# Kernel tuning notes

Measured on AMD Instinct MI355X. Metric: run time of the kernel, lower is better.

The kernel has to match this reference:

```python
import jax, jax.numpy as jnp
import numpy as np

H = 768      # hidden_size
NH = 12      # num_attention_heads
DH = H // NH # attention_head_size
FF = 3072    # intermediate_size
E = 4        # n_expert
B, S = 8, 512
EPS = 1e-12


def _layernorm(x, g, b):
    mu = jnp.mean(x, axis=-1, keepdims=True)
    var = jnp.var(x, axis=-1, keepdims=True)
    return (x - mu) * jax.lax.rsqrt(var + EPS) * g + b


def _expert_linear(x, W, b, expert_idx):
    # W: [E, in, out], b: [E, out]; gather per-sample expert weights, then batched GEMM.
    # Mathematically identical to running every expert then slicing (single_select_fwd).
    Wg = W[expert_idx]            # [B, in, out]
    bg = b[expert_idx]            # [B, out]
    return jnp.einsum('bsi,bio->bso', x, Wg) + bg[:, None, :]


def setup_inputs() -> dict:
    key = jax.random.key(0)
    ks = jax.random.split(key, 16)
    sc = 0.02
    inp = {
        'hidden_states': jax.random.normal(ks[0], (B, S, H), jnp.float32),
        'expert_idx': jax.random.randint(ks[1], (B,), 0, E, jnp.int64) if jax.config.read('jax_enable_x64') else jax.random.randint(ks[1], (B,), 0, E).astype(jnp.int32),
        'attention_mask': jnp.zeros((B, 1, 1, S), jnp.float32),
        'Wq': sc * jax.random.normal(ks[2], (E, H, H), jnp.float32),
        'bq': jnp.zeros((E, H), jnp.float32),
        'Wk': sc * jax.random.normal(ks[3], (E, H, H), jnp.float32),
        'bk': jnp.zeros((E, H), jnp.float32),
        'Wv': sc * jax.random.normal(ks[4], (E, H, H), jnp.float32),
        'bv': jnp.zeros((E, H), jnp.float32),
        'Wo': sc * jax.random.normal(ks[5], (E, H, H), jnp.float32),
        'bo': jnp.zeros((E, H), jnp.float32),
        'ln1_g': jnp.ones((H,), jnp.float32),
        'ln1_b': jnp.zeros((H,), jnp.float32),
        'Wi': sc * jax.random.normal(ks[6], (E, H, FF), jnp.float32),
        'bi': jnp.zeros((E, FF), jnp.float32),
        'Wout': sc * jax.random.normal(ks[7], (E, FF, H), jnp.float32),
        'bout': jnp.zeros((E, H), jnp.float32),
        'ln2_g': jnp.ones((H,), jnp.float32),
        'ln2_b': jnp.zeros((H,), jnp.float32),
    }
    return inp


def reference(hidden_states, expert_idx, attention_mask, Wq, bq, Wk, bk, Wv, bv,
              Wo, bo, ln1_g, ln1_b, Wi, bi, Wout, bout, ln2_g, ln2_b):
    b, s, h = hidden_states.shape
    # --- MoE self-attention (per-sample expert QKV) ---
    q = _expert_linear(hidden_states, Wq, bq, expert_idx).reshape(b, s, NH, DH).transpose(0, 2, 1, 3)
    k = _expert_linear(hidden_states, Wk, bk, expert_idx).reshape(b, s, NH, DH).transpose(0, 2, 1, 3)
    v = _expert_linear(hidden_states, Wv, bv, expert_idx).reshape(b, s, NH, DH).transpose(0, 2, 1, 3)
    scores = jnp.einsum('bhqd,bhkd->bhqk', q, k) / np.sqrt(DH).astype(np.float32)
    scores = scores + attention_mask
    probs = jax.nn.softmax(scores, axis=-1)
    ctx = jnp.einsum('bhqk,bhkd->bhqd', probs, v).transpose(0, 2, 1, 3).reshape(b, s, h)
    # --- MoE self-output: dense + residual + LN ---
    attn_out = _expert_linear(ctx, Wo, bo, expert_idx)
    x = _layernorm(attn_out + hidden_states, ln1_g, ln1_b)
    # --- MoE FFN: intermediate (GELU) + output + residual + LN ---
    hmid = jax.nn.gelu(_expert_linear(x, Wi, bi, expert_idx), approximate=False)
    ffn = _expert_linear(hmid, Wout, bout, expert_idx)
    return _layernorm(ffn + x, ln2_g, ln2_b)
```

## Files before the change

### kernel.cpp

```cpp
#include <hip/hip_runtime.h>
#include <cstdint>
#include <cstddef>

constexpr int CB  = 8;
constexpr int CS  = 512;
constexpr int CH  = 768;
constexpr int CNH = 12;
constexpr int CDH = 64;
constexpr int CFF = 3072;
constexpr int CE  = 4;
constexpr int C3H = 3 * CH;

using f32x4  = __attribute__((ext_vector_type(4))) float;
using bf16x8 = __attribute__((ext_vector_type(8))) short;

__device__ __forceinline__ short f2bf(float x) {
  union { float f; uint32_t u; } v; v.f = x;
  return (short)((v.u + 0x7fffu + ((v.u >> 16) & 1u)) >> 16);
}

__device__ __forceinline__ void gload_lds16(const void* g, void* l) {
  __builtin_amdgcn_global_load_lds((const __attribute__((address_space(1))) void*)g,
                                   (__attribute__((address_space(3))) void*)l,
                                   16, 0, 0);
}

#define VMCNT(n)  asm volatile("s_waitcnt vmcnt(" #n ")" ::: "memory")
#define SCHEDB()  __builtin_amdgcn_sched_barrier(0)

__global__ void cvt_bf16_kernel(const float* __restrict__ in, short* __restrict__ out, int n4) {
  int i = blockIdx.x * blockDim.x + threadIdx.x;
  if (i < n4) {
    float4 v = ((const float4*)in)[i];
    short4 o;
    o.x = f2bf(v.x); o.y = f2bf(v.y); o.z = f2bf(v.z); o.w = f2bf(v.w);
    ((short4*)out)[i] = o;
  }
}

__device__ __forceinline__ bool expert_used(const int* __restrict__ eidx, int e) {
  bool u = false;
#pragma unroll
  for (int s = 0; s < CB; ++s) u |= (eidx[s] == e);
  return u;
}

__device__ __forceinline__ void tpose_body(const float* __restrict__ Wb,
                                           short* __restrict__ Wtb, int K, int N) {
  __shared__ __align__(16) short Ts[64 * 68];
  const int n0 = blockIdx.x * 64, k0 = blockIdx.y * 64;
  const int t  = threadIdx.x;
  const int tn = t & 15, tk = t >> 4;
#pragma unroll
  for (int p = 0; p < 4; ++p) {
    int k = k0 + p * 16 + tk;
    float4 v = *(const float4*)(Wb + (size_t)k * N + n0 + tn * 4);
#pragma unroll
    for (int j = 0; j < 4; ++j)
      Ts[(tn * 4 + j) * 68 + p * 16 + tk] = f2bf(((const float*)&v)[j]);
  }
  __syncthreads();
#pragma unroll
  for (int p = 0; p < 4; ++p) {
    int n = n0 + p * 16 + tk;
    uint2 o = *(const uint2*)(Ts + (p * 16 + tk) * 68 + tn * 4);
    *(uint2*)(Wtb + (size_t)n * K + k0 + tn * 4) = o;
  }
}

__global__ void tpose_cvt_kernel(const float* __restrict__ W, short* __restrict__ Wt,
                                 const int* __restrict__ eidx, int K, int N) {
  const int e = blockIdx.z;
  if (!expert_used(eidx, e)) return;
  tpose_body(W + (size_t)e * K * N, Wt + (size_t)e * K * N, K, N);
}

__global__ void tpose4_kernel(const float* __restrict__ Wq, const float* __restrict__ Wk,
                              const float* __restrict__ Wv, const float* __restrict__ Wo,
                              const int* __restrict__ eidx,
                              short* __restrict__ Wqkvt, short* __restrict__ Wot) {
  const int z = blockIdx.z, e = z >> 2, m = z & 3;
  if (!expert_used(eidx, e)) return;
  const float* W = (m == 0) ? Wq : (m == 1) ? Wk : (m == 2) ? Wv : Wo;
  const float* Wb = W + (size_t)e * CH * CH;
  short* dst = (m == 3) ? (Wot + (size_t)e * CH * CH)
                        : (Wqkvt + ((size_t)e * C3H + m * CH) * CH);
  tpose_body(Wb, dst, CH, CH);
}

__global__ void qkv_bias_kernel(const float* __restrict__ bq, const float* __restrict__ bk,
                                const float* __restrict__ bv, float* __restrict__ dst) {
  int i = blockIdx.x * 256 + threadIdx.x;
  if (i >= CE * C3H) return;
  int e = i / C3H, r = i % C3H;
  int m = r / CH, c = r % CH;
  const float* s = (m == 0) ? bq : (m == 1) ? bk : bv;
  dst[i] = s[e * CH + c];
}

template <int BM, int BN, int TPB, int K, int NTN, int KSPLIT, int ACT, bool OB16>
__global__ __launch_bounds__(TPB, 2)
void gemm4_kernel(const short* __restrict__ A, const short* __restrict__ Wt,
                  const float* __restrict__ bias, const int* __restrict__ eidx,
                  char* __restrict__ out,
                  size_t wtExpStride, int biasStride, int outLd, size_t outKsStride) {
  constexpr int WAVES = TPB / 64;
  constexpr int WARPS_N = BN / 64, WARPS_M = WAVES / WARPS_N;
  constexpr int WM = BM / WARPS_M, MI = WM / 16;
  constexpr int NT = K / KSPLIT / 64;
  constexpr int JC = 4096 / BM;
  constexpr int MTS = CS / BM;
  __shared__ __align__(16) short As[2][BM * 64];
  __shared__ __align__(16) short Bs[2][BN * 64];
  const int t = threadIdx.x, w = t >> 6, l = t & 63, lr = l & 15, lg = l >> 4;

  int exv[CB];
#pragma unroll
  for (int s = 0; s < CB; ++s) exv[s] = eidx[s];
  uint32_t epack = 0;
#pragma unroll
  for (int s = 0; s < CB; ++s) epack |= (uint32_t)exv[s] << (2 * s);
  int c0 = 0, c1 = 0, c2 = 0;
#pragma unroll
  for (int s = 0; s < CB; ++s) {
    c0 += (exv[s] == 0); c1 += (exv[s] == 1); c2 += (exv[s] == 2);
  }
  int p0 = 0, p1 = c0, p2 = c0 + c1, p3 = c0 + c1 + c2;
  uint32_t sortedPack = 0;
#pragma unroll
  for (int s = 0; s < CB; ++s) {
    int e = exv[s];
    int p = (e == 0) ? p0 : (e == 1) ? p1 : (e == 2) ? p2 : p3;
    sortedPack |= (uint32_t)s << (4 * p);
    p0 += (e == 0); p1 += (e == 1); p2 += (e == 2); p3 += (e == 3);
  }
  const int chunk = (int)gridDim.x >> 3;
  const int W_ = ((int)blockIdx.x & 7) * chunk + ((int)blockIdx.x >> 3);
  const int ks = W_ / (JC * NTN);
  const int r1 = W_ - ks * (JC * NTN);
  const int j  = r1 / NTN, nt = r1 - j * NTN;
  const int sample = (int)((sortedPack >> (4 * (j / MTS))) & 7);
  const int jj = j % MTS;
  const int e  = (int)((epack >> (2 * sample)) & 3);
  const int mrow0 = sample * CS + jj * BM;
  const int kBase = ks * NT * 64;

  const int srow = t >> 3;
  const int gcol = (((t & 7) ^ ((t >> 3) & 7)) * 8);
  const short* aSrc = A + (size_t)(mrow0 + srow) * K + kBase + gcol;
  const short* bSrc = Wt + (size_t)e * wtExpStride + (size_t)(nt * BN + srow) * K + kBase + gcol;
  constexpr int RPI = TPB / 8;
  const size_t issStride = (size_t)RPI * K;

  const int wrow = (w / WARPS_N) * WM, wn = (w % WARPS_N) * 64;
  int aoff[2][MI], boff[2][4];
#pragma unroll
  for (int kk = 0; kk < 2; ++kk) {
    const int slot = (kk * 4 + lg) ^ (lr & 7);
#pragma unroll
    for (int mi = 0; mi < MI; ++mi)
      aoff[kk][mi] = (wrow + mi * 16 + lr) * 64 + slot * 8;
#pragma unroll
    for (int ni = 0; ni < 4; ++ni)
      boff[kk][ni] = (wn + ni * 16 + lr) * 64 + slot * 8;
  }

  f32x4 acc[MI][4] = {};

  auto STAGE = [&](int buf, int kt) {
    const short* as = aSrc + (size_t)kt * 64;
#pragma unroll
    for (int i = 0; i < BM / RPI; ++i)
      gload_lds16(as + i * issStride, &As[buf][i * TPB * 8 + t * 8]);
    const short* bs = bSrc + (size_t)kt * 64;
#pragma unroll
    for (int i = 0; i < BN / RPI; ++i)
      gload_lds16(bs + i * issStride, &Bs[buf][i * TPB * 8 + t * 8]);
  };

  STAGE(0, 0);
  for (int kt = 0; kt < NT; ++kt) {
    const int buf = kt & 1;
    if (kt + 1 < NT) { STAGE(buf ^ 1, kt + 1); VMCNT(8); }
    else             { VMCNT(0); }
    __builtin_amdgcn_s_barrier();
    SCHEDB();
    bf16x8 af[2][MI], bfr[2][4];
#pragma unroll
    for (int kk = 0; kk < 2; ++kk) {
#pragma unroll
      for (int ni = 0; ni < 4; ++ni) bfr[kk][ni] = *(const bf16x8*)(&Bs[buf][boff[kk][ni]]);
#pragma unroll
      for (int mi = 0; mi < MI; ++mi) af[kk][mi] = *(const bf16x8*)(&As[buf][aoff[kk][mi]]);
    }
    __builtin_amdgcn_s_setprio(1);
#pragma unroll
    for (int kk = 0; kk < 2; ++kk)
#pragma unroll
      for (int mi = 0; mi < MI; ++mi)
#pragma unroll
        for (int ni = 0; ni < 4; ++ni)
          acc[mi][ni] = __builtin_amdgcn_mfma_f32_16x16x32_bf16(af[kk][mi], bfr[kk][ni],
                                                                acc[mi][ni], 0, 0, 0);
    __builtin_amdgcn_s_setprio(0);
    __builtin_amdgcn_s_barrier();
    SCHEDB();
  }

  float* outF = (float*)out + (size_t)ks * outKsStride;
#pragma unroll
  for (int ni = 0; ni < 4; ++ni) {
    const int col = nt * BN + wn + ni * 16 + lr;
    const float bv = bias ? bias[e * biasStride + col] : 0.0f;
#pragma unroll
    for (int mi = 0; mi < MI; ++mi) {
      const int row0 = mrow0 + wrow + mi * 16 + lg * 4;
#pragma unroll
      for (int r = 0; r < 4; ++r) {
        float v = acc[mi][ni][r] + bv;
        if (ACT == 1) v = 0.5f * v * (1.0f + erff(v * 0.70710678118654752f));
        if (OB16) ((short*)out)[(size_t)(row0 + r) * outLd + col] = f2bf(v);
        else      outF[(size_t)(row0 + r) * outLd + col] = v;
      }
    }
  }
}

__global__ void attn_kernel(const short* __restrict__ QKV, const float* __restrict__ mask,
                            short* __restrict__ ctx) {
  __shared__ __align__(16) short Vt[2][64 * 40];
  __shared__ __align__(16) short Pt[4][2][16 * 40];
  const int bh = blockIdx.x;
  const int b = bh / CNH, h = bh % CNH;
  const int qt = blockIdx.y;
  const int t = threadIdx.x, w = t >> 6, l = t & 63, lr = l & 15, lg = l >> 4;

  const size_t bS = (size_t)b * CS;
  const short* Qh = QKV + bS * C3H + h * CDH;
  const short* Kh = Qh + CH;
  const short* Vh = Qh + 2 * CH;
  const float* mrow = mask + bS;

  const int qrow = qt * 64 + w * 16 + lr;
  bf16x8 qa[2];
  qa[0] = *(const bf16x8*)(Qh + (size_t)qrow * C3H + lg * 8);
  qa[1] = *(const bf16x8*)(Qh + (size_t)qrow * C3H + 32 + lg * 8);

  f32x4 o[4] = {};
  float lp[4] = {0.f, 0.f, 0.f, 0.f};

  const int dh = t & 63, kg = t >> 6;
  {
    short v8[8];
#pragma unroll
    for (int j = 0; j < 8; ++j) v8[j] = Vh[(size_t)(kg * 8 + j) * C3H + dh];
    uint32_t p0 = (uint32_t)(uint16_t)v8[0] | ((uint32_t)(uint16_t)v8[1] << 16);
    uint32_t p1 = (uint32_t)(uint16_t)v8[2] | ((uint32_t)(uint16_t)v8[3] << 16);
    uint32_t p2 = (uint32_t)(uint16_t)v8[4] | ((uint32_t)(uint16_t)v8[5] << 16);
    uint32_t p3 = (uint32_t)(uint16_t)v8[6] | ((uint32_t)(uint16_t)v8[7] << 16);
    uint4 pk = {p0, p1, p2, p3};
    *(uint4*)(&Vt[0][dh * 40 + kg * 8]) = pk;
  }

  for (int tt = 0; tt < CS / 32; ++tt) {
    const int k0 = tt * 32;
    __syncthreads();

    f32x4 sacc[2] = {};
#pragma unroll
    for (int n = 0; n < 2; ++n) {
      bf16x8 kb0 = *(const bf16x8*)(Kh + (size_t)(k0 + n * 16 + lr) * C3H + lg * 8);
      bf16x8 kb1 = *(const bf16x8*)(Kh + (size_t)(k0 + n * 16 + lr) * C3H + 32 + lg * 8);
      sacc[n] = __builtin_amdgcn_mfma_f32_16x16x32_bf16(qa[0], kb0, sacc[n], 0, 0, 0);
      sacc[n] = __builtin_amdgcn_mfma_f32_16x16x32_bf16(qa[1], kb1, sacc[n], 0, 0, 0);
    }

    if (tt + 1 < CS / 32) {
      const int k1 = k0 + 32;
      short v8[8];
#pragma unroll
      for (int j = 0; j < 8; ++j) v8[j] = Vh[(size_t)(k1 + kg * 8 + j) * C3H + dh];
      uint32_t p0 = (uint32_t)(uint16_t)v8[0] | ((uint32_t)(uint16_t)v8[1] << 16);
      uint32_t p1 = (uint32_t)(uint16_t)v8[2] | ((uint32_t)(uint16_t)v8[3] << 16);
      uint32_t p2 = (uint32_t)(uint16_t)v8[4] | ((uint32_t)(uint16_t)v8[5] << 16);
      uint32_t p3 = (uint32_t)(uint16_t)v8[6] | ((uint32_t)(uint16_t)v8[7] << 16);
      uint4 pk = {p0, p1, p2, p3};
      *(uint4*)(&Vt[(tt + 1) & 1][dh * 40 + kg * 8]) = pk;
    }

    const int pb = tt & 1;
#pragma unroll
    for (int n = 0; n < 2; ++n) {
      float mv = mrow[k0 + n * 16 + lr];
#pragma unroll
      for (int r = 0; r < 4; ++r) {
        float s = sacc[n][r] * 0.125f + mv;
        float e = __expf(s);
        lp[r] += e;
        Pt[w][pb][(lg * 4 + r) * 40 + n * 16 + lr] = f2bf(e);
      }
    }

    bf16x8 pa = *(const bf16x8*)(&Pt[w][pb][lr * 40 + lg * 8]);
#pragma unroll
    for (int d = 0; d < 4; ++d) {
      bf16x8 vbf = *(const bf16x8*)(&Vt[tt & 1][(d * 16 + lr) * 40 + lg * 8]);
      o[d] = __builtin_amdgcn_mfma_f32_16x16x32_bf16(pa, vbf, o[d], 0, 0, 0);
    }
  }

#pragma unroll
  for (int r = 0; r < 4; ++r) {
    float s = lp[r];
    s += __shfl_xor(s, 1); s += __shfl_xor(s, 2);
    s += __shfl_xor(s, 4); s += __shfl_xor(s, 8);
    lp[r] = 1.0f / s;
  }
#pragma unroll
  for (int d = 0; d < 4; ++d)
#pragma unroll
    for (int r = 0; r < 4; ++r) {
      int row = qt * 64 + w * 16 + lg * 4 + r;
      ctx[(bS + row) * CH + h * CDH + d * 16 + lr] = f2bf(o[d][r] * lp[r]);
    }
}

__global__ void ln_kernel(const float* __restrict__ xin, const float* __restrict__ res,
                          const float* __restrict__ g, const float* __restrict__ bta,
                          float* __restrict__ out32, short* __restrict__ out16) {
  const int row = blockIdx.x;
  const int l = threadIdx.x;
  const float* xr = xin + (size_t)row * CH;
  const float* rr = res + (size_t)row * CH;
  float4 v[3];
  float sum = 0.f, ss = 0.f;
#pragma unroll
  for (int j = 0; j < 3; ++j) {
    float4 a = *(const float4*)(xr + j * 256 + l * 4);
    float4 b = *(const float4*)(rr + j * 256 + l * 4);
    a.x += b.x; a.y += b.y; a.z += b.z; a.w += b.w;
    v[j] = a;
    sum += a.x + a.y + a.z + a.w;
    ss  += a.x * a.x + a.y * a.y + a.z * a.z + a.w * a.w;
  }
#pragma unroll
  for (int m = 1; m < 64; m <<= 1) { sum += __shfl_xor(sum, m); ss += __shfl_xor(ss, m); }
  const float mean = sum * (1.0f / CH);
  const float var  = ss * (1.0f / CH) - mean * mean;
  const float rstd = rsqrtf(var + 1e-12f);
#pragma unroll
  for (int j = 0; j < 3; ++j) {
    float4 gg = *(const float4*)(g   + j * 256 + l * 4);
    float4 bb = *(const float4*)(bta + j * 256 + l * 4);
    float4 a = v[j], y;
    y.x = (a.x - mean) * rstd * gg.x + bb.x;
    y.y = (a.y - mean) * rstd * gg.y + bb.y;
    y.z = (a.z - mean) * rstd * gg.z + bb.z;
    y.w = (a.w - mean) * rstd * gg.w + bb.w;
    *(float4*)(out32 + (size_t)row * CH + j * 256 + l * 4) = y;
    if (out16) {
      short4 o;
      o.x = f2bf(y.x); o.y = f2bf(y.y); o.z = f2bf(y.z); o.w = f2bf(y.w);
      *(short4*)(out16 + (size_t)row * CH + j * 256 + l * 4) = o;
    }
  }
}

__global__ void ln2_kernel(const float* __restrict__ p0, const float* __restrict__ p1,
                           const float* __restrict__ res,
                           const float* __restrict__ bout, const int* __restrict__ eidx,
                           const float* __restrict__ g, const float* __restrict__ bta,
                           float* __restrict__ out) {
  const int row = blockIdx.x;
  const int l = threadIdx.x;
  const int e = eidx[row >> 9];
  const float* xr0 = p0 + (size_t)row * CH;
  const float* xr1 = p1 + (size_t)row * CH;
  const float* rr  = res + (size_t)row * CH;
  const float* bo  = bout + (size_t)e * CH;
  float4 v[3];
  float sum = 0.f, ss = 0.f;
#pragma unroll
  for (int j = 0; j < 3; ++j) {
    float4 a = *(const float4*)(xr0 + j * 256 + l * 4);
    float4 c = *(const float4*)(xr1 + j * 256 + l * 4);
    float4 b = *(const float4*)(rr + j * 256 + l * 4);
    float4 bb = *(const float4*)(bo + j * 256 + l * 4);
    a.x += c.x + b.x + bb.x; a.y += c.y + b.y + bb.y;
    a.z += c.z + b.z + bb.z; a.w += c.w + b.w + bb.w;
    v[j] = a;
    sum += a.x + a.y + a.z + a.w;
    ss  += a.x * a.x + a.y * a.y + a.z * a.z + a.w * a.w;
  }
#pragma unroll
  for (int m = 1; m < 64; m <<= 1) { sum += __shfl_xor(sum, m); ss += __shfl_xor(ss, m); }
  const float mean = sum * (1.0f / CH);
  const float var  = ss * (1.0f / CH) - mean * mean;
  const float rstd = rsqrtf(var + 1e-12f);
#pragma unroll
  for (int j = 0; j < 3; ++j) {
    float4 gg = *(const float4*)(g   + j * 256 + l * 4);
    float4 bb = *(const float4*)(bta + j * 256 + l * 4);
    float4 a = v[j], y;
    y.x = (a.x - mean) * rstd * gg.x + bb.x;
    y.y = (a.y - mean) * rstd * gg.y + bb.y;
    y.z = (a.z - mean) * rstd * gg.z + bb.z;
    y.w = (a.w - mean) * rstd * gg.w + bb.w;
    *(float4*)(out + (size_t)row * CH + j * 256 + l * 4) = y;
  }
}

extern "C" void kernel_launch(void* const* d_in, const int* in_sizes, int n_in,
                              void* d_out, int out_size, void* d_ws, size_t ws_size,
                              hipStream_t stream) {
  (void)in_sizes; (void)n_in; (void)out_size; (void)ws_size;
  const float* hidden = (const float*)d_in[0];
  const int*   eidx   = (const int*)d_in[1];
  const float* mask   = (const float*)d_in[2];
  const float* Wq   = (const float*)d_in[3];
  const float* bq   = (const float*)d_in[4];
  const float* Wk   = (const float*)d_in[5];
  const float* bk   = (const float*)d_in[6];
  const float* Wv   = (const float*)d_in[7];
  const float* bv   = (const float*)d_in[8];
  const float* Wo   = (const float*)d_in[9];
  const float* bo   = (const float*)d_in[10];
  const float* ln1g = (const float*)d_in[11];
  const float* ln1b = (const float*)d_in[12];
  const float* Wi   = (const float*)d_in[13];
  const float* bi   = (const float*)d_in[14];
  const float* Wout = (const float*)d_in[15];
  const float* bout = (const float*)d_in[16];
  const float* ln2g = (const float*)d_in[17];
  const float* ln2b = (const float*)d_in[18];

  char* ws = (char*)d_ws;
  size_t off = 0;
  auto alloc = [&](size_t bytes) {
    void* p = ws + off;
    off += (bytes + 255) & ~(size_t)255;
    return p;
  };
  const size_t M = (size_t)CB * CS;
  short* Xb    = (short*)alloc(M * CH * 2);
  char*  Rbig  = (char*)alloc(M * CFF * 2);
  char*  Rcx   = (char*)alloc(M * CH * 4);
  float* ffnp  = (float*)alloc(2 * M * CH * 4);
  float* qkvbias = (float*)alloc(CE * C3H * 4);
  short* Wqkvt = (short*)alloc((size_t)CE * C3H * CH * 2);
  short* Wot   = (short*)alloc((size_t)CE * CH * CH * 2);
  short* Wit   = (short*)alloc((size_t)CE * CH * CFF * 2);
  short* Wo2t  = (short*)alloc((size_t)CE * CFF * CH * 2);
  short* QKVb     = (short*)Rbig;
  short* hmid     = (short*)Rbig;
  short* ctxb     = (short*)Rcx;
  float* x1       = (float*)Rcx;
  short* x1b      = Xb;
  float* attn_out = (float*)Wqkvt;

  const int n4 = (int)(M * CH / 4);
  cvt_bf16_kernel<<<(n4 + 255) / 256, 256, 0, stream>>>(hidden, Xb, n4);
  tpose4_kernel<<<dim3(CH / 64, CH / 64, 4 * CE), 256, 0, stream>>>(Wq, Wk, Wv, Wo, eidx, Wqkvt, Wot);
  tpose_cvt_kernel<<<dim3(CFF / 64, CH / 64, CE), 256, 0, stream>>>(Wi, Wit, eidx, CH, CFF);
  tpose_cvt_kernel<<<dim3(CH / 64, CFF / 64, CE), 256, 0, stream>>>(Wout, Wo2t, eidx, CFF, CH);
  qkv_bias_kernel<<<(CE * C3H + 255) / 256, 256, 0, stream>>>(bq, bk, bv, qkvbias);

  gemm4_kernel<256, 256, 512, CH, 9, 1, 0, true><<<144, 512, 0, stream>>>(
      Xb, Wqkvt, qkvbias, eidx, (char*)QKVb, (size_t)C3H * CH, C3H, C3H, 0);
  attn_kernel<<<dim3(CB * CNH, CS / 64), 256, 0, stream>>>(QKVb, mask, ctxb);
  gemm4_kernel<128, 128, 256, CH, 6, 1, 0, false><<<192, 256, 0, stream>>>(
      ctxb, Wot, bo, eidx, (char*)attn_out, (size_t)CH * CH, CH, CH, 0);
  ln_kernel<<<(int)M, 64, 0, stream>>>(attn_out, hidden, ln1g, ln1b, x1, x1b);
  gemm4_kernel<256, 256, 512, CH, 12, 1, 1, true><<<192, 512, 0, stream>>>(
      x1b, Wit, bi, eidx, (char*)hmid, (size_t)CH * CFF, CFF, CFF, 0);
  gemm4_kernel<128, 128, 256, CFF, 6, 2, 0, false><<<384, 256, 0, stream>>>(
      hmid, Wo2t, nullptr, eidx, (char*)ffnp, (size_t)CFF * CH, CH, CH, M * CH);
  ln2_kernel<<<(int)M, 64, 0, stream>>>(ffnp, ffnp + M * CH, x1, bout, eidx,
                                        ln2g, ln2b, (float*)d_out);
}
```

Baseline: 201.4 us.

## Use 128x128 tiles for all GEMMs and split-K the attention output projection

Fixes every expert GEMM at 128x128 tiles with 256 threads, dropping the 256x256/512-thread config for the QKV and intermediate GEMMs. This gives 576 and 768 workgroups instead of 144 and 192, for better CU occupancy and load balance. The attention output projection now uses split-K by 2 into partial buffers, and a merged LN kernel sums the partials, residual and expert bias for both layernorms. The smaller tiles lower data reuse per tile, and the split adds extra fp32 partial writes and reads.

Result: slower. 205.8 us (+2.2%).

```diff
diff --git a/kernel.cpp b/kernel.cpp
--- a/kernel.cpp
+++ b/kernel.cpp
@@ -98,15 +98,14 @@
   dst[i] = s[e * CH + c];
 }
 
-template <int BM, int BN, int TPB, int K, int NTN, int KSPLIT, int ACT, bool OB16>
-__global__ __launch_bounds__(TPB, 2)
-void gemm4_kernel(const short* __restrict__ A, const short* __restrict__ Wt,
+template <int K, int NTN, int KSPLIT, int ACT, bool OB16>
+__global__ __launch_bounds__(256, 2)
+void gemm5_kernel(const short* __restrict__ A, const short* __restrict__ Wt,
                   const float* __restrict__ bias, const int* __restrict__ eidx,
                   char* __restrict__ out,
                   size_t wtExpStride, int biasStride, int outLd, size_t outKsStride) {
-  constexpr int WAVES = TPB / 64;
-  constexpr int WARPS_N = BN / 64, WARPS_M = WAVES / WARPS_N;
-  constexpr int WM = BM / WARPS_M, MI = WM / 16;
+  constexpr int BM = 128, BN = 128, TPB = 256;
+  constexpr int MI = 4;
   constexpr int NT = K / KSPLIT / 64;
   constexpr int JC = 4096 / BM;
   constexpr int MTS = CS / BM;
@@ -152,7 +151,7 @@
   constexpr int RPI = TPB / 8;
   const size_t issStride = (size_t)RPI * K;
 
-  const int wrow = (w / WARPS_N) * WM, wn = (w % WARPS_N) * 64;
+  const int wrow = (w >> 1) * 64, wn = (w & 1) * 64;
   int aoff[2][MI], boff[2][4];
 #pragma unroll
   for (int kk = 0; kk < 2; ++kk) {
@@ -170,11 +169,11 @@
   auto STAGE = [&](int buf, int kt) {
     const short* as = aSrc + (size_t)kt * 64;
 #pragma unroll
-    for (int i = 0; i < BM / RPI; ++i)
+    for (int i = 0; i < 4; ++i)
       gload_lds16(as + i * issStride, &As[buf][i * TPB * 8 + t * 8]);
     const short* bs = bSrc + (size_t)kt * 64;
 #pragma unroll
-    for (int i = 0; i < BN / RPI; ++i)
+    for (int i = 0; i < 4; ++i)
       gload_lds16(bs + i * issStride, &Bs[buf][i * TPB * 8 + t * 8]);
   };
 
@@ -325,20 +324,28 @@
     }
 }
 
-__global__ void ln_kernel(const float* __restrict__ xin, const float* __restrict__ res,
-                          const float* __restrict__ g, const float* __restrict__ bta,
-                          float* __restrict__ out32, short* __restrict__ out16) {
+__global__ void ln12_kernel(const float* __restrict__ p0, const float* __restrict__ p1,
+                            const float* __restrict__ res,
+                            const float* __restrict__ btab, const int* __restrict__ eidx,
+                            const float* __restrict__ g, const float* __restrict__ bta,
+                            float* __restrict__ out32, short* __restrict__ out16) {
   const int row = blockIdx.x;
   const int l = threadIdx.x;
-  const float* xr = xin + (size_t)row * CH;
-  const float* rr = res + (size_t)row * CH;
+  const int e = eidx[row >> 9];
+  const float* xr0 = p0 + (size_t)row * CH;
+  const float* xr1 = p1 + (size_t)row * CH;
+  const float* rr  = res + (size_t)row * CH;
+  const float* bo  = btab + (size_t)e * CH;
   float4 v[3];
   float sum = 0.f, ss = 0.f;
 #pragma unroll
   for (int j = 0; j < 3; ++j) {
-    float4 a = *(const float4*)(xr + j * 256 + l * 4);
+    float4 a = *(const float4*)(xr0 + j * 256 + l * 4);
+    float4 c = *(const float4*)(xr1 + j * 256 + l * 4);
     float4 b = *(const float4*)(rr + j * 256 + l * 4);
-    a.x += b.x; a.y += b.y; a.z += b.z; a.w += b.w;
+    float4 bb = *(const float4*)(bo + j * 256 + l * 4);
+    a.x += c.x + b.x + bb.x; a.y += c.y + b.y + bb.y;
+    a.z += c.z + b.z + bb.z; a.w += c.w + b.w + bb.w;
     v[j] = a;
     sum += a.x + a.y + a.z + a.w;
     ss  += a.x * a.x + a.y * a.y + a.z * a.z + a.w * a.w;
@@ -363,50 +370,6 @@
       o.x = f2bf(y.x); o.y = f2bf(y.y); o.z = f2bf(y.z); o.w = f2bf(y.w);
       *(short4*)(out16 + (size_t)row * CH + j * 256 + l * 4) = o;
     }
-  }
-}
-
-__global__ void ln2_kernel(const float* __restrict__ p0, const float* __restrict__ p1,
-                           const float* __restrict__ res,
-                           const float* __restrict__ bout, const int* __restrict__ eidx,
-                           const float* __restrict__ g, const float* __restrict__ bta,
-                           float* __restrict__ out) {
-  const int row = blockIdx.x;
-  const int l = threadIdx.x;
-  const int e = eidx[row >> 9];
-  const float* xr0 = p0 + (size_t)row * CH;
-  const float* xr1 = p1 + (size_t)row * CH;
-  const float* rr  = res + (size_t)row * CH;
-  const float* bo  = bout + (size_t)e * CH;
-  float4 v[3];
-  float sum = 0.f, ss = 0.f;
-#pragma unroll
-  for (int j = 0; j < 3; ++j) {
-    float4 a = *(const float4*)(xr0 + j * 256 + l * 4);
-    float4 c = *(const float4*)(xr1 + j * 256 + l * 4);
-    float4 b = *(const float4*)(rr + j * 256 + l * 4);
-    float4 bb = *(const float4*)(bo + j * 256 + l * 4);
-    a.x += c.x + b.x + bb.x; a.y += c.y + b.y + bb.y;
-    a.z += c.z + b.z + bb.z; a.w += c.w + b.w + bb.w;
-    v[j] = a;
-    sum += a.x + a.y + a.z + a.w;
-    ss  += a.x * a.x + a.y * a.y + a.z * a.z + a.w * a.w;
-  }
-#pragma unroll
-  for (int m = 1; m < 64; m <<= 1) { sum += __shfl_xor(sum, m); ss += __shfl_xor(ss, m); }
-  const float mean = sum * (1.0f / CH);
-  const float var  = ss * (1.0f / CH) - mean * mean;
-  const float rstd = rsqrtf(var + 1e-12f);
-#pragma unroll
-  for (int j = 0; j < 3; ++j) {
-    float4 gg = *(const float4*)(g   + j * 256 + l * 4);
-    float4 bb = *(const float4*)(bta + j * 256 + l * 4);
-    float4 a = v[j], y;
-    y.x = (a.x - mean) * rstd * gg.x + bb.x;
-    y.y = (a.y - mean) * rstd * gg.y + bb.y;
-    y.z = (a.z - mean) * rstd * gg.z + bb.z;
-    y.w = (a.w - mean) * rstd * gg.w + bb.w;
-    *(float4*)(out + (size_t)row * CH + j * 256 + l * 4) = y;
   }
 }
 
@@ -445,18 +408,17 @@
   short* Xb    = (short*)alloc(M * CH * 2);
   char*  Rbig  = (char*)alloc(M * CFF * 2);
   char*  Rcx   = (char*)alloc(M * CH * 4);
-  float* ffnp  = (float*)alloc(2 * M * CH * 4);
+  float* parts = (float*)alloc(2 * M * CH * 4);
   float* qkvbias = (float*)alloc(CE * C3H * 4);
   short* Wqkvt = (short*)alloc((size_t)CE * C3H * CH * 2);
   short* Wot   = (short*)alloc((size_t)CE * CH * CH * 2);
   short* Wit   = (short*)alloc((size_t)CE * CH * CFF * 2);
   short* Wo2t  = (short*)alloc((size_t)CE * CFF * CH * 2);
-  short* QKVb     = (short*)Rbig;
-  short* hmid     = (short*)Rbig;
-  short* ctxb     = (short*)Rcx;
-  float* x1       = (float*)Rcx;
-  short* x1b      = Xb;
-  float* attn_out = (float*)Wqkvt;
+  short* QKVb = (short*)Rbig;
+  short* hmid = (short*)Rbig;
+  short* ctxb = (short*)Rcx;
+  float* x1   = (float*)Rcx;
+  short* x1b  = Xb;
 
   const int n4 = (int)(M * CH / 4);
   cvt_bf16_kernel<<<(n4 + 255) / 256, 256, 0, stream>>>(hidden, Xb, n4);
@@ -465,16 +427,17 @@
   tpose_cvt_kernel<<<dim3(CH / 64, CFF / 64, CE), 256, 0, stream>>>(Wout, Wo2t, eidx, CFF, CH);
   qkv_bias_kernel<<<(CE * C3H + 255) / 256, 256, 0, stream>>>(bq, bk, bv, qkvbias);
 
-  gemm4_kernel<256, 256, 512, CH, 9, 1, 0, true><<<144, 512, 0, stream>>>(
+  gemm5_kernel<CH, 18, 1, 0, true><<<576, 256, 0, stream>>>(
       Xb, Wqkvt, qkvbias, eidx, (char*)QKVb, (size_t)C3H * CH, C3H, C3H, 0);
   attn_kernel<<<dim3(CB * CNH, CS / 64), 256, 0, stream>>>(QKVb, mask, ctxb);
-  gemm4_kernel<128, 128, 256, CH, 6, 1, 0, false><<<192, 256, 0, stream>>>(
-      ctxb, Wot, bo, eidx, (char*)attn_out, (size_t)CH * CH, CH, CH, 0);
-  ln_kernel<<<(int)M, 64, 0, stream>>>(attn_out, hidden, ln1g, ln1b, x1, x1b);
-  gemm4_kernel<256, 256, 512, CH, 12, 1, 1, true><<<192, 512, 0, stream>>>(
+  gemm5_kernel<CH, 6, 2, 0, false><<<384, 256, 0, stream>>>(
+      ctxb, Wot, nullptr, eidx, (char*)parts, (size_t)CH * CH, CH, CH, M * CH);
+  ln12_kernel<<<(int)M, 64, 0, stream>>>(parts, parts + M * CH, hidden, bo, eidx,
+                                         ln1g, ln1b, x1, x1b);
+  gemm5_kernel<CH, 24, 1, 1, true><<<768, 256, 0, stream>>>(
       x1b, Wit, bi, eidx, (char*)hmid, (size_t)CH * CFF, CFF, CFF, 0);
-  gemm4_kernel<128, 128, 256, CFF, 6, 2, 0, false><<<384, 256, 0, stream>>>(
-      hmid, Wo2t, nullptr, eidx, (char*)ffnp, (size_t)CFF * CH, CH, CH, M * CH);
-  ln2_kernel<<<(int)M, 64, 0, stream>>>(ffnp, ffnp + M * CH, x1, bout, eidx,
-                                        ln2g, ln2b, (float*)d_out);
-}
+  gemm5_kernel<CFF, 6, 2, 0, false><<<384, 256, 0, stream>>>(
+      hmid, Wo2t, nullptr, eidx, (char*)parts, (size_t)CFF * CH, CH, CH, M * CH);
+  ln12_kernel<<<(int)M, 64, 0, stream>>>(parts, parts + M * CH, x1, bout, eidx,
+                                         ln2g, ln2b, (float*)d_out, nullptr);
+}
```
